# Optimization experiments

Measured on AMD Instinct MI355X. Metric: run time of the kernel, lower is better.

Reference implementation:

```python
import jax, jax.numpy as jnp
import numpy as np

TW, NV, EMB, LAYERS = 25, 4, 128, 6
N, E = 65536, 262144
T_MAX = 16.0
EPS = 1e-5

def silu(x):
    return x * jax.nn.sigmoid(x)

def setup_inputs() -> dict:
    key = jax.random.key(0)
    ks = iter(jax.random.split(key, 32))
    def nrm(shape, scale=0.05):
        return jax.random.normal(next(ks), shape, jnp.float32) * scale
    inp = {}
    inp['x'] = jax.random.normal(next(ks), (N, TW), jnp.float32)
    inp['pos'] = jax.random.uniform(next(ks), (N, 1), jnp.float32)
    inp['variables'] = jax.random.uniform(next(ks), (N, NV), jnp.float32)
    inp['dt'] = jnp.full((1,), 0.1, jnp.float32)
    inp['edge_index'] = jax.random.randint(next(ks), (2, E), 0, N)
    inp['enc_W1'] = nrm((TW + NV + 1, EMB)); inp['enc_b1'] = jnp.zeros((EMB,), jnp.float32)
    inp['enc_W2'] = nrm((EMB, EMB));         inp['enc_b2'] = jnp.zeros((EMB,), jnp.float32)
    dmsg = 2 * EMB + TW + 1 + NV   # 286: x_i,x_j,u_i-u_j,pos_i-pos_j,vars_i
    dupd = 2 * EMB + NV            # 260: x, aggregated message, vars
    inp['msg_W1'] = nrm((LAYERS, dmsg, EMB)); inp['msg_b1'] = jnp.zeros((LAYERS, EMB), jnp.float32)
    inp['msg_W2'] = nrm((LAYERS, EMB, EMB));  inp['msg_b2'] = jnp.zeros((LAYERS, EMB), jnp.float32)
    inp['upd_W1'] = nrm((LAYERS, dupd, EMB)); inp['upd_b1'] = jnp.zeros((LAYERS, EMB), jnp.float32)
    inp['upd_W2'] = nrm((LAYERS, EMB, EMB));  inp['upd_b2'] = jnp.zeros((LAYERS, EMB), jnp.float32)
    inp['dec_W1'] = nrm((8, 1, 16)); inp['dec_b1'] = jnp.zeros((8,), jnp.float32)
    inp['dec_W2'] = nrm((1, 8, 14)); inp['dec_b2'] = jnp.zeros((1,), jnp.float32)
    return inp

def reference(x, pos, variables, dt, edge_index,
              enc_W1, enc_b1, enc_W2, enc_b2,
              msg_W1, msg_b1, msg_W2, msg_b2,
              upd_W1, upd_b1, upd_W2, upd_b2,
              dec_W1, dec_b1, dec_W2, dec_b2):
    vars3 = variables[:, :3]              # alpha, beta, gamma
    t = variables[:, 3:4] / T_MAX         # normalized time
    p = pos / jnp.max(pos)                # graph.pos /= pos.max()
    inp0 = jnp.concatenate([x, p, t, vars3], axis=-1)  # [N, 30]
    h = silu(silu(inp0 @ enc_W1 + enc_b1) @ enc_W2 + enc_b2)  # [N, EMB]

    src, dst = edge_index[0], edge_index[1]  # x_j = src, x_i = dst (source_to_target)
    deg = jax.ops.segment_sum(jnp.ones((E,), jnp.float32), dst, num_segments=N)
    inv_deg = (1.0 / jnp.maximum(deg, 1.0))[:, None]

    for l in range(LAYERS):
        m_in = jnp.concatenate(
            [h[dst], h[src], x[dst] - x[src], p[dst] - p[src], variables[dst]], axis=-1)
        m = silu(m_in @ msg_W1[l] + msg_b1[l])
        m = silu(m @ msg_W2[l] + msg_b2[l])                      # [E, EMB]
        agg = jax.ops.segment_sum(m, dst, num_segments=N) * inv_deg  # mean aggr
        u = silu(jnp.concatenate([h, agg, variables], axis=-1) @ upd_W1[l] + upd_b1[l])
        u = silu(u @ upd_W2[l] + upd_b2[l])
        h_new = h + u  # in_features == out_features -> residual
        # PyG InstanceNorm (affine=False), single graph (batch all zeros)
        mu = jnp.mean(h_new, axis=0, keepdims=True)
        var = jnp.var(h_new, axis=0, keepdims=True)
        h = (h_new - mu) * jax.lax.rsqrt(var + EPS)

    # decoder: Conv1d(1->8, k=16, s=3) -> SiLU -> Conv1d(8->1, k=14, s=1)
    z = h[:, None, :]  # [N, 1, EMB]
    z = jax.lax.conv_general_dilated(z, dec_W1, (3,), 'VALID',
                                     dimension_numbers=('NCH', 'OIH', 'NCH')) + dec_b1[None, :, None]
    z = silu(z)
    z = jax.lax.conv_general_dilated(z, dec_W2, (1,), 'VALID',
                                     dimension_numbers=('NCH', 'OIH', 'NCH')) + dec_b2[None, :, None]
    diff = z[:, 0, :]  # [N, TW]
    dtc = dt[0] * jnp.arange(1, TW + 1, dtype=jnp.float32)  # cumsum of dt*ones
    return jnp.tile(x[:, -1:], (1, TW)) + dtc[None, :] * diff
```

## Files before the change

### kernel.cpp

```cpp
#include <hip/hip_runtime.h>
#include <math.h>

#define N_NODES 65536
#define N_EDGES 262144
#define N_LAYERS 6
#define T_MAX_F 16.0f
#define EPS_F 1e-5f

typedef float  f32x4  __attribute__((ext_vector_type(4)));
typedef __bf16 bf16x8 __attribute__((ext_vector_type(8)));
typedef __bf16 bf16x4 __attribute__((ext_vector_type(4)));

__device__ __forceinline__ float silu_f(float v){
    return v / (1.0f + __expf(-v));
}

__device__ __forceinline__ f32x4 mfma16(bf16x8 a, bf16x8 b, f32x4 c){
    return __builtin_amdgcn_mfma_f32_16x16x32_bf16(a, b, c, 0, 0, 0);
}

#define PK_RA (6 * 20480)
#define PK_RB (6 * 20480)
#define PK_M2 (6 * 16384)
#define PK_U1 (6 * 36864)
#define PK_U2 (6 * 16384)
#define PK_TOTAL (PK_RA + PK_RB + PK_M2 + PK_U1 + PK_U2)

__global__ __launch_bounds__(256) void k_pack(const float* __restrict__ msgW1, const float* __restrict__ msgW2,
                                              const float* __restrict__ updW1, const float* __restrict__ updW2,
                                              __bf16* __restrict__ out){
    int pg = blockIdx.x * 256 + threadIdx.x;
    if (pg >= PK_TOTAL) return;
    int p = pg;
    int mode; const float* W; int perL;
    if (p < PK_RA){ mode = 0; W = msgW1; perL = 20480; }
    else if ((p -= PK_RA) < PK_RB){ mode = 1; W = msgW1; perL = 20480; }
    else if ((p -= PK_RB) < PK_M2){ mode = 2; W = msgW2; perL = 16384; }
    else if ((p -= PK_M2) < PK_U1){ mode = 3; W = updW1; perL = 36864; }
    else { p -= PK_U1; mode = 4; W = updW2; perL = 16384; }
    int l = p / perL, q = p % perL;
    int elem = q & 7, lane = (q >> 3) & 63, cb = (q >> 9) & 7, kb = q >> 12;
    int col = cb * 16 + (lane & 15);
    int k = kb * 32 + ((lane >> 4) << 3) + elem;
    float v = 0.0f;
    if (mode == 0){
        int r = -1;
        if (k < 128) r = k;
        else if (k < 153) r = 256 + (k - 128);
        else if (k == 153) r = 281;
        else if (k < 158) r = 282 + (k - 154);
        if (r >= 0) v = W[(size_t)l * 286 * 128 + (size_t)r * 128 + col];
    } else if (mode == 1){
        if (k < 128) v = W[(size_t)l * 286 * 128 + (size_t)(128 + k) * 128 + col];
        else if (k < 153) v = -W[(size_t)l * 286 * 128 + (size_t)(256 + (k - 128)) * 128 + col];
        else if (k == 153) v = -W[(size_t)l * 286 * 128 + (size_t)281 * 128 + col];
    } else {
        int Kreal = (mode == 3) ? 260 : 128;
        if (k < Kreal) v = W[(size_t)l * Kreal * 128 + (size_t)k * 128 + col];
    }
    out[pg] = (__bf16)v;
}

__global__ __launch_bounds__(256) void k_max(const float* __restrict__ pos, unsigned* __restrict__ outmax){
    __shared__ float s[256];
    int tid = threadIdx.x;
    float m = 0.0f;
    for (int i = blockIdx.x * 256 + tid; i < N_NODES; i += 256 * 256)
        m = fmaxf(m, pos[i]);
    s[tid] = m;
    __syncthreads();
    for (int off = 128; off > 0; off >>= 1){
        if (tid < off) s[tid] = fmaxf(s[tid], s[tid + off]);
        __syncthreads();
    }
    if (tid == 0) atomicMax(outmax, __float_as_uint(s[0]));
}

__global__ __launch_bounds__(256) void k_deg(const int* __restrict__ dst, int* __restrict__ deg){
    int i = blockIdx.x * 256 + threadIdx.x;
    if (i < N_EDGES) atomicAdd(deg + dst[i], 1);
}

__global__ __launch_bounds__(256) void k_prep(const float* __restrict__ pos, const unsigned* __restrict__ maxp,
                                              const int* __restrict__ deg,
                                              float* __restrict__ p, float* __restrict__ invdeg){
    int i = blockIdx.x * 256 + threadIdx.x;
    if (i < N_NODES){
        float mp = __uint_as_float(*maxp);
        p[i] = pos[i] / mp;
        invdeg[i] = 1.0f / fmaxf((float)deg[i], 1.0f);
    }
}

__global__ __launch_bounds__(256) void k_scan1(const int* __restrict__ deg, int* __restrict__ csum){
    __shared__ int s[256];
    int c = blockIdx.x, t = threadIdx.x;
    s[t] = deg[c * 256 + t];
    __syncthreads();
    for (int o = 128; o > 0; o >>= 1){ if (t < o) s[t] += s[t + o]; __syncthreads(); }
    if (t == 0) csum[c] = s[0];
}

__global__ __launch_bounds__(256) void k_scan2(const int* __restrict__ csum, int* __restrict__ coff){
    __shared__ int s[256];
    int t = threadIdx.x;
    s[t] = csum[t];
    __syncthreads();
    for (int o = 1; o < 256; o <<= 1){
        int v = (t >= o) ? s[t - o] : 0;
        __syncthreads();
        s[t] += v;
        __syncthreads();
    }
    coff[t] = s[t] - csum[t];
}

__global__ __launch_bounds__(256) void k_scan3(const int* __restrict__ deg, const int* __restrict__ coff,
                                               int* __restrict__ cursor){
    __shared__ int s[256];
    int c = blockIdx.x, t = threadIdx.x;
    int d = deg[c * 256 + t];
    s[t] = d;
    __syncthreads();
    for (int o = 1; o < 256; o <<= 1){
        int v = (t >= o) ? s[t - o] : 0;
        __syncthreads();
        s[t] += v;
        __syncthreads();
    }
    cursor[c * 256 + t] = coff[c] + s[t] - d;
}

__global__ __launch_bounds__(256) void k_scatter(const int* __restrict__ esrc, const int* __restrict__ edst,
                                                 int* __restrict__ cursor,
                                                 int* __restrict__ ssrcS, int* __restrict__ sdstS){
    int e = blockIdx.x * 256 + threadIdx.x;
    if (e < N_EDGES){
        int d = edst[e];
        int slot = atomicAdd(cursor + d, 1);
        ssrcS[slot] = esrc[e];
        sdstS[slot] = d;
    }
}

__device__ __forceinline__ void gemm44(const float* A, int lda, const float* __restrict__ W,
                                       int kq_begin, int kq_end, int r0, int c0, float acc[4][4]){
    for (int kq = kq_begin; kq < kq_end; ++kq){
        int k = kq * 4;
        float a[4][4], w[4][4];
        #pragma unroll
        for (int i = 0; i < 4; ++i){
            float4 v = *(const float4*)(A + (r0 + i) * lda + k);
            a[i][0] = v.x; a[i][1] = v.y; a[i][2] = v.z; a[i][3] = v.w;
        }
        #pragma unroll
        for (int kk = 0; kk < 4; ++kk){
            float4 v = *(const float4*)(W + (k + kk) * 128 + c0);
            w[kk][0] = v.x; w[kk][1] = v.y; w[kk][2] = v.z; w[kk][3] = v.w;
        }
        #pragma unroll
        for (int kk = 0; kk < 4; ++kk)
            #pragma unroll
            for (int i = 0; i < 4; ++i)
                #pragma unroll
                for (int j = 0; j < 4; ++j)
                    acc[i][j] = fmaf(a[i][kk], w[kk][j], acc[i][j]);
    }
}

__global__ __launch_bounds__(256) void k_enc(const float* __restrict__ x, const float* __restrict__ p,
                                             const float* __restrict__ vars,
                                             const float* __restrict__ W1, const float* __restrict__ b1,
                                             const float* __restrict__ W2, const float* __restrict__ b2,
                                             float* __restrict__ hA){
    __shared__ __align__(16) float sin_[32 * 32];
    __shared__ __align__(16) float sw1[32 * 128];
    __shared__ __align__(16) float sy[32 * 128];
    int tid = threadIdx.x;
    int n0 = blockIdx.x * 32;
    for (int i = tid; i < 32 * 32; i += 256){
        int e = i >> 5, k = i & 31;
        int node = n0 + e;
        float v;
        if (k < 25)       v = x[node * 25 + k];
        else if (k == 25) v = p[node];
        else if (k == 26) v = vars[node * 4 + 3] * (1.0f / T_MAX_F);
        else if (k < 30)  v = vars[node * 4 + (k - 27)];
        else              v = 0.0f;
        sin_[e * 32 + k] = v;
    }
    for (int i = tid; i < 32 * 128; i += 256){
        int r = i >> 7;
        sw1[i] = (r < 30) ? W1[i] : 0.0f;
    }
    __syncthreads();
    int c0 = (tid & 31) * 4, r0 = (tid >> 5) * 4;
    float acc[4][4] = {};
    gemm44(sin_, 32, sw1, 0, 8, r0, c0, acc);
    float4 bv = *(const float4*)(b1 + c0);
    float b_[4] = {bv.x, bv.y, bv.z, bv.w};
    #pragma unroll
    for (int i = 0; i < 4; ++i){
        float4 o;
        o.x = silu_f(acc[i][0] + b_[0]);
        o.y = silu_f(acc[i][1] + b_[1]);
        o.z = silu_f(acc[i][2] + b_[2]);
        o.w = silu_f(acc[i][3] + b_[3]);
        *(float4*)(sy + (r0 + i) * 128 + c0) = o;
    }
    __syncthreads();
    float acc2[4][4] = {};
    gemm44(sy, 128, W2, 0, 32, r0, c0, acc2);
    float4 b2v = *(const float4*)(b2 + c0);
    float bb[4] = {b2v.x, b2v.y, b2v.z, b2v.w};
    #pragma unroll
    for (int i = 0; i < 4; ++i){
        float4 o;
        o.x = silu_f(acc2[i][0] + bb[0]);
        o.y = silu_f(acc2[i][1] + bb[1]);
        o.z = silu_f(acc2[i][2] + bb[2]);
        o.w = silu_f(acc2[i][3] + bb[3]);
        *(float4*)(hA + (size_t)(n0 + r0 + i) * 128 + c0) = o;
    }
}

__global__ __launch_bounds__(256) void k_npre(const float* __restrict__ hA, const float* __restrict__ x,
                                              const float* __restrict__ p, const float* __restrict__ vars,
                                              const float* __restrict__ mu, const float* __restrict__ istd,
                                              int apply_ln,
                                              const __bf16* __restrict__ Wra, const __bf16* __restrict__ Wrb,
                                              const float* __restrict__ b1,
                                              float* __restrict__ raO, __bf16* __restrict__ rbO,
                                              float* __restrict__ aggZ, float* __restrict__ saccZ){
    __shared__ __align__(16) __bf16 sA[10 * 64 * 8];
    __shared__ __align__(16) float sOut[32 * 264];
    int tid = threadIdx.x;
    int n0 = blockIdx.x * 32;
    {
        float4 z4 = {0.f, 0.f, 0.f, 0.f};
        #pragma unroll
        for (int it = 0; it < 4; ++it){
            int i = tid + it * 256;
            int e = i >> 5, ch = i & 31;
            *(float4*)(aggZ + (size_t)(n0 + e) * 128 + ch * 4) = z4;
        }
        if (blockIdx.x == 0) saccZ[tid] = 0.f;
    }
    #pragma unroll
    for (int it = 0; it < 3; ++it){
        int j = tid + it * 256;
        if (j < 640){
            int f = j >> 6, lane = j & 63;
            int kb = f >> 1, mt = f & 1;
            int e = (lane & 15) + mt * 16, kh = lane >> 4;
            int node = n0 + e;
            bf16x8 o;
            if (kb < 4){
                int k0 = kb * 32 + kh * 8;
                float4 v0 = *(const float4*)(hA + (size_t)node * 128 + k0);
                float4 v1 = *(const float4*)(hA + (size_t)node * 128 + k0 + 4);
                if (apply_ln){
                    float4 m0 = *(const float4*)(mu + k0),   m1 = *(const float4*)(mu + k0 + 4);
                    float4 s0 = *(const float4*)(istd + k0), s1 = *(const float4*)(istd + k0 + 4);
                    v0.x = (v0.x - m0.x) * s0.x; v0.y = (v0.y - m0.y) * s0.y;
                    v0.z = (v0.z - m0.z) * s0.z; v0.w = (v0.w - m0.w) * s0.w;
                    v1.x = (v1.x - m1.x) * s1.x; v1.y = (v1.y - m1.y) * s1.y;
                    v1.z = (v1.z - m1.z) * s1.z; v1.w = (v1.w - m1.w) * s1.w;
                }
                o[0] = (__bf16)v0.x; o[1] = (__bf16)v0.y; o[2] = (__bf16)v0.z; o[3] = (__bf16)v0.w;
                o[4] = (__bf16)v1.x; o[5] = (__bf16)v1.y; o[6] = (__bf16)v1.z; o[7] = (__bf16)v1.w;
            } else {
                #pragma unroll
                for (int jj = 0; jj < 8; ++jj){
                    int fk = kh * 8 + jj;
                    float v;
                    if (fk < 25)       v = x[node * 25 + fk];
                    else if (fk == 25) v = p[node];
                    else if (fk < 30)  v = vars[node * 4 + (fk - 26)];
                    else               v = 0.0f;
                    o[jj] = (__bf16)v;
                }
            }
            *(bf16x8*)(sA + (f * 64 + lane) * 8) = o;
        }
    }
    __syncthreads();
    int w = tid >> 6, lane = tid & 63;
    int clo = lane & 15, rhi = lane >> 4;
    f32x4 z = {0.f, 0.f, 0.f, 0.f};
    f32x4 aR[2][2] = {{z, z}, {z, z}};
    f32x4 aB[2][2] = {{z, z}, {z, z}};
    #pragma unroll
    for (int kb = 0; kb < 5; ++kb){
        bf16x8 a0 = *(bf16x8*)(sA + ((kb * 2 + 0) * 64 + lane) * 8);
        bf16x8 a1 = *(bf16x8*)(sA + ((kb * 2 + 1) * 64 + lane) * 8);
        bf16x8 wr0 = *(const bf16x8*)(Wra + (size_t)((kb * 8 + 2 * w)     * 64 + lane) * 8);
        bf16x8 wr1 = *(const bf16x8*)(Wra + (size_t)((kb * 8 + 2 * w + 1) * 64 + lane) * 8);
        bf16x8 wb0 = *(const bf16x8*)(Wrb + (size_t)((kb * 8 + 2 * w)     * 64 + lane) * 8);
        bf16x8 wb1 = *(const bf16x8*)(Wrb + (size_t)((kb * 8 + 2 * w + 1) * 64 + lane) * 8);
        aR[0][0] = mfma16(a0, wr0, aR[0][0]);
        aR[0][1] = mfma16(a0, wr1, aR[0][1]);
        aR[1][0] = mfma16(a1, wr0, aR[1][0]);
        aR[1][1] = mfma16(a1, wr1, aR[1][1]);
        aB[0][0] = mfma16(a0, wb0, aB[0][0]);
        aB[0][1] = mfma16(a0, wb1, aB[0][1]);
        aB[1][0] = mfma16(a1, wb0, aB[1][0]);
        aB[1][1] = mfma16(a1, wb1, aB[1][1]);
    }
    #pragma unroll
    for (int nf = 0; nf < 2; ++nf){
        int col = (2 * w + nf) * 16 + clo;
        float bv = b1[col];
        #pragma unroll
        for (int mt = 0; mt < 2; ++mt)
            #pragma unroll
            for (int i = 0; i < 4; ++i){
                int e = mt * 16 + rhi * 4 + i;
                sOut[e * 264 + col]       = aR[mt][nf][i] + bv;
                sOut[e * 264 + 128 + col] = aB[mt][nf][i];
            }
    }
    __syncthreads();
    #pragma unroll
    for (int it = 0; it < 4; ++it){
        int j = tid + it * 256;
        int row = j >> 5, c8 = j & 31;
        const float* src = sOut + row * 264 + c8 * 8;
        if (c8 < 16){
            float4 v0 = *(const float4*)(src);
            float4 v1 = *(const float4*)(src + 4);
            float* dstp = raO + (size_t)(n0 + row) * 128 + c8 * 8;
            *(float4*)(dstp)     = v0;
            *(float4*)(dstp + 4) = v1;
        } else {
            bf16x8 o;
            #pragma unroll
            for (int t = 0; t < 8; ++t) o[t] = (__bf16)src[t];
            *(bf16x8*)(rbO + (size_t)(n0 + row) * 128 + (c8 - 16) * 8) = o;
        }
    }
}

__global__ __launch_bounds__(256) void k_edge3(const float* __restrict__ ra, const __bf16* __restrict__ rb,
                                               const int* __restrict__ ssrcS, const int* __restrict__ sdstS,
                                               const __bf16* __restrict__ Wp2, const float* __restrict__ bias2,
                                               float* __restrict__ agg){
    __shared__ __align__(16) unsigned char smem[64 * 128 * 4];
    __shared__ int sd[64], ss[64];
    __bf16* sA   = (__bf16*)smem;
    float*  msum = (float*)smem;
    int tid = threadIdx.x;
    int e0 = blockIdx.x * 64;
    if (tid < 64){ sd[tid] = sdstS[e0 + tid]; ss[tid] = ssrcS[e0 + tid]; }
    __syncthreads();
    #pragma unroll
    for (int it = 0; it < 4; ++it){
        int j = tid + it * 256;
        int f = j >> 6, lane = j & 63;
        int kb = f >> 2, mt = f & 3;
        int e = (lane & 15) + mt * 16;
        int k0 = kb * 32 + (lane >> 4) * 8;
        const float* rap = ra + (size_t)sd[e] * 128 + k0;
        float4 v0 = *(const float4*)(rap);
        float4 v1 = *(const float4*)(rap + 4);
        bf16x8 vb = *(const bf16x8*)(rb + (size_t)ss[e] * 128 + k0);
        bf16x8 o;
        o[0] = (__bf16)silu_f(v0.x + (float)vb[0]);
        o[1] = (__bf16)silu_f(v0.y + (float)vb[1]);
        o[2] = (__bf16)silu_f(v0.z + (float)vb[2]);
        o[3] = (__bf16)silu_f(v0.w + (float)vb[3]);
        o[4] = (__bf16)silu_f(v1.x + (float)vb[4]);
        o[5] = (__bf16)silu_f(v1.y + (float)vb[5]);
        o[6] = (__bf16)silu_f(v1.z + (float)vb[6]);
        o[7] = (__bf16)silu_f(v1.w + (float)vb[7]);
        *(bf16x8*)(sA + (f * 64 + lane) * 8) = o;
    }
    __syncthreads();
    int w = tid >> 6, lane = tid & 63;
    int cb0 = 2 * w, clo = lane & 15, rhi = lane >> 4;
    f32x4 z = {0.f, 0.f, 0.f, 0.f};
    f32x4 acc[4][2] = {{z, z}, {z, z}, {z, z}, {z, z}};
    #pragma unroll
    for (int kb = 0; kb < 4; ++kb){
        bf16x8 a0 = *(bf16x8*)(sA + ((kb * 4 + 0) * 64 + lane) * 8);
        bf16x8 a1 = *(bf16x8*)(sA + ((kb * 4 + 1) * 64 + lane) * 8);
        bf16x8 a2 = *(bf16x8*)(sA + ((kb * 4 + 2) * 64 + lane) * 8);
        bf16x8 a3 = *(bf16x8*)(sA + ((kb * 4 + 3) * 64 + lane) * 8);
        bf16x8 w0 = *(const bf16x8*)(Wp2 + (size_t)((kb * 8 + cb0)     * 64 + lane) * 8);
        bf16x8 w1 = *(const bf16x8*)(Wp2 + (size_t)((kb * 8 + cb0 + 1) * 64 + lane) * 8);
        acc[0][0] = mfma16(a0, w0, acc[0][0]);
        acc[0][1] = mfma16(a0, w1, acc[0][1]);
        acc[1][0] = mfma16(a1, w0, acc[1][0]);
        acc[1][1] = mfma16(a1, w1, acc[1][1]);
        acc[2][0] = mfma16(a2, w0, acc[2][0]);
        acc[2][1] = mfma16(a2, w1, acc[2][1]);
        acc[3][0] = mfma16(a3, w0, acc[3][0]);
        acc[3][1] = mfma16(a3, w1, acc[3][1]);
    }
    __syncthreads();
    #pragma unroll
    for (int nf = 0; nf < 2; ++nf){
        int col = (cb0 + nf) * 16 + clo;
        float bv = bias2[col];
        #pragma unroll
        for (int mt = 0; mt < 4; ++mt)
            #pragma unroll
            for (int i = 0; i < 4; ++i){
                int row = mt * 16 + rhi * 4 + i;
                msum[row * 128 + col] = silu_f(acc[mt][nf][i] + bv);
            }
    }
    __syncthreads();
    int col = tid & 127, half = tid >> 7;
    int base = half * 32;
    float run = 0.0f;
    for (int r = 0; r < 32; ++r){
        int row = base + r;
        run += msum[row * 128 + col];
        bool flush = (r == 31) || (sd[row + 1] != sd[row]);
        if (flush){
            atomicAdd(agg + (size_t)sd[row] * 128 + col, run);
            run = 0.0f;
        }
    }
}

__global__ __launch_bounds__(256) void k_upd_m(float* __restrict__ hA, const float* __restrict__ agg,
                                               const float* __restrict__ vars, const float* __restrict__ invdeg,
                                               const float* __restrict__ mu, const float* __restrict__ istd,
                                               int apply_ln,
                                               const __bf16* __restrict__ Wp1, const float* __restrict__ bias1,
                                               const __bf16* __restrict__ Wp2, const float* __restrict__ bias2,
                                               float* __restrict__ sacc, float* __restrict__ qacc){
    __shared__ __align__(16) __bf16 sA1[36 * 64 * 8];
    __bf16* zb = sA1;
    int tid = threadIdx.x;
    int n0 = blockIdx.x * 64;
    #pragma unroll
    for (int it = 0; it < 9; ++it){
        int idx = tid + it * 256;
        int f = idx >> 6, lane = idx & 63;
        int kb = f >> 2, mt = f & 3;
        int row = (lane & 15) + mt * 16;
        int node = n0 + row;
        int k0 = kb * 32 + ((lane >> 4) << 3);
        bf16x8 o;
        if (k0 < 128){
            float4 v0 = *(const float4*)(hA + (size_t)node * 128 + k0);
            float4 v1 = *(const float4*)(hA + (size_t)node * 128 + k0 + 4);
            if (apply_ln){
                float4 m0 = *(const float4*)(mu + k0),   m1 = *(const float4*)(mu + k0 + 4);
                float4 s0 = *(const float4*)(istd + k0), s1 = *(const float4*)(istd + k0 + 4);
                v0.x = (v0.x - m0.x) * s0.x; v0.y = (v0.y - m0.y) * s0.y;
                v0.z = (v0.z - m0.z) * s0.z; v0.w = (v0.w - m0.w) * s0.w;
                v1.x = (v1.x - m1.x) * s1.x; v1.y = (v1.y - m1.y) * s1.y;
                v1.z = (v1.z - m1.z) * s1.z; v1.w = (v1.w - m1.w) * s1.w;
            }
            o[0] = (__bf16)v0.x; o[1] = (__bf16)v0.y; o[2] = (__bf16)v0.z; o[3] = (__bf16)v0.w;
            o[4] = (__bf16)v1.x; o[5] = (__bf16)v1.y; o[6] = (__bf16)v1.z; o[7] = (__bf16)v1.w;
        } else if (k0 < 256){
            int g0 = k0 - 128;
            float4 v0 = *(const float4*)(agg + (size_t)node * 128 + g0);
            float4 v1 = *(const float4*)(agg + (size_t)node * 128 + g0 + 4);
            float s = invdeg[node];
            o[0] = (__bf16)(v0.x * s); o[1] = (__bf16)(v0.y * s); o[2] = (__bf16)(v0.z * s); o[3] = (__bf16)(v0.w * s);
            o[4] = (__bf16)(v1.x * s); o[5] = (__bf16)(v1.y * s); o[6] = (__bf16)(v1.z * s); o[7] = (__bf16)(v1.w * s);
        } else {
            int fk = k0 - 256;
            #pragma unroll
            for (int jj = 0; jj < 8; ++jj){
                int kk = fk + jj;
                o[jj] = (__bf16)((kk < 4) ? vars[(size_t)node * 4 + kk] : 0.0f);
            }
        }
        *(bf16x8*)(sA1 + (size_t)idx * 8) = o;
    }
    __syncthreads();
    int w = tid >> 6, lane = tid & 63;
    int cb0 = 2 * w, clo = lane & 15, rhi = lane >> 4;
    f32x4 z = {0.f, 0.f, 0.f, 0.f};
    f32x4 acc[4][2] = {{z, z}, {z, z}, {z, z}, {z, z}};
    #pragma unroll
    for (int kb = 0; kb < 9; ++kb){
        bf16x8 w0 = *(const bf16x8*)(Wp1 + (size_t)((kb * 8 + cb0)     * 64 + lane) * 8);
        bf16x8 w1 = *(const bf16x8*)(Wp1 + (size_t)((kb * 8 + cb0 + 1) * 64 + lane) * 8);
        #pragma unroll
        for (int mt = 0; mt < 4; ++mt){
            bf16x8 a = *(bf16x8*)(sA1 + ((kb * 4 + mt) * 64 + lane) * 8);
            acc[mt][0] = mfma16(a, w0, acc[mt][0]);
            acc[mt][1] = mfma16(a, w1, acc[mt][1]);
        }
    }
    __syncthreads();
    #pragma unroll
    for (int nf = 0; nf < 2; ++nf){
        int col = (cb0 + nf) * 16 + clo;
        float bv = bias1[col];
        #pragma unroll
        for (int mt = 0; mt < 4; ++mt)
            #pragma unroll
            for (int i = 0; i < 4; ++i){
                int row = mt * 16 + rhi * 4 + i;
                zb[row * 152 + col] = (__bf16)silu_f(acc[mt][nf][i] + bv);
            }
    }
    __syncthreads();
    f32x4 acc2[4][2] = {{z, z}, {z, z}, {z, z}, {z, z}};
    #pragma unroll
    for (int kb = 0; kb < 4; ++kb){
        bf16x8 w0 = *(const bf16x8*)(Wp2 + (size_t)((kb * 8 + cb0)     * 64 + lane) * 8);
        bf16x8 w1 = *(const bf16x8*)(Wp2 + (size_t)((kb * 8 + cb0 + 1) * 64 + lane) * 8);
        int k0 = kb * 32 + ((lane >> 4) << 3);
        #pragma unroll
        for (int mt = 0; mt < 4; ++mt){
            int row = (lane & 15) + mt * 16;
            bf16x8 a = *(bf16x8*)(zb + row * 152 + k0);
            acc2[mt][0] = mfma16(a, w0, acc2[mt][0]);
            acc2[mt][1] = mfma16(a, w1, acc2[mt][1]);
        }
    }
    float sm[2] = {0.f, 0.f}, sq[2] = {0.f, 0.f};
    #pragma unroll
    for (int nf = 0; nf < 2; ++nf){
        int col = (cb0 + nf) * 16 + clo;
        float bv = bias2[col];
        float muv = apply_ln ? mu[col] : 0.0f;
        float sdv = apply_ln ? istd[col] : 1.0f;
        #pragma unroll
        for (int mt = 0; mt < 4; ++mt)
            #pragma unroll
            for (int i = 0; i < 4; ++i){
                int row = mt * 16 + rhi * 4 + i;
                size_t idx = (size_t)(n0 + row) * 128 + col;
                float u = silu_f(acc2[mt][nf][i] + bv);
                float hln = (hA[idx] - muv) * sdv;
                float hv = hln + u;
                hA[idx] = hv;
                sm[nf] += hv; sq[nf] += hv * hv;
            }
    }
    #pragma unroll
    for (int nf = 0; nf < 2; ++nf){
        float s = sm[nf], q = sq[nf];
        s += __shfl_xor(s, 16); q += __shfl_xor(q, 16);
        s += __shfl_xor(s, 32); q += __shfl_xor(q, 32);
        if (rhi == 0){
            int col = (cb0 + nf) * 16 + clo;
            atomicAdd(sacc + col, s);
            atomicAdd(qacc + col, q);
        }
    }
}

__global__ __launch_bounds__(128) void k_statfin(const float* __restrict__ sacc, const float* __restrict__ qacc,
                                                 float* __restrict__ mu, float* __restrict__ istd){
    int c = threadIdx.x;
    float m = sacc[c] * (1.0f / N_NODES);
    float v = qacc[c] * (1.0f / N_NODES) - m * m;
    mu[c] = m;
    istd[c] = rsqrtf(v + EPS_F);
}

#define DECNB 16
__global__ __launch_bounds__(256) void k_dec(const float* __restrict__ h, const float* __restrict__ x,
                                             const float* __restrict__ dt,
                                             const float* __restrict__ W1, const float* __restrict__ b1,
                                             const float* __restrict__ W2, const float* __restrict__ b2,
                                             const float* __restrict__ mu, const float* __restrict__ istd,
                                             float* __restrict__ out){
    __shared__ __align__(16) float sh[DECNB * 132];
    __shared__ __align__(16) float so[DECNB * 312];
    __shared__ float pp[DECNB * 8 * 26];
    __shared__ float sw1[128], sw2[112], sb1[8];
    int tid = threadIdx.x;
    int n0 = blockIdx.x * DECNB;
    for (int i = tid; i < DECNB * 32; i += 256){
        int g = i >> 5, chunk = i & 31;
        float4 v = *(const float4*)(h + (size_t)(n0 + g) * 128 + chunk * 4);
        float4 m = *(const float4*)(mu + chunk * 4);
        float4 s = *(const float4*)(istd + chunk * 4);
        v.x = (v.x - m.x) * s.x; v.y = (v.y - m.y) * s.y;
        v.z = (v.z - m.z) * s.z; v.w = (v.w - m.w) * s.w;
        *(float4*)(sh + g * 132 + chunk * 4) = v;
    }
    if (tid < 128) sw1[tid] = W1[tid];
    else if (tid < 240) sw2[tid - 128] = W2[tid - 128];
    if (tid < 8) sb1[tid] = b1[tid];
    __syncthreads();
    {
        int g = tid >> 4, c = (tid >> 1) & 7, jh = tid & 1;
        int j0 = jh * 19;
        float w[16];
        #pragma unroll
        for (int k = 0; k < 16; ++k) w[k] = sw1[c * 16 + k];
        float bc = sb1[c];
        float win[16];
        #pragma unroll
        for (int k = 0; k < 16; ++k) win[k] = sh[g * 132 + 3 * j0 + k];
        #pragma unroll
        for (int j = 0; j < 19; ++j){
            float a = bc;
            #pragma unroll
            for (int k = 0; k < 16; ++k) a = fmaf(win[k], w[k], a);
            so[g * 312 + c * 38 + j0 + j] = silu_f(a);
            if (j < 18){
                #pragma unroll
                for (int k = 0; k < 13; ++k) win[k] = win[k + 3];
                int base = g * 132 + 3 * (j0 + j + 1) + 13;
                win[13] = sh[base]; win[14] = sh[base + 1]; win[15] = sh[base + 2];
            }
        }
    }
    __syncthreads();
    {
        int g = tid >> 4, c = (tid >> 1) & 7, th = tid & 1;
        int t0 = th * 13;
        int nt = th ? 12 : 13;
        float w[14];
        #pragma unroll
        for (int k = 0; k < 14; ++k) w[k] = sw2[c * 14 + k];
        float win[14];
        #pragma unroll
        for (int k = 0; k < 14; ++k) win[k] = so[g * 312 + c * 38 + t0 + k];
        #pragma unroll
        for (int t = 0; t < 13; ++t){
            if (t < nt){
                float a = 0.0f;
                #pragma unroll
                for (int k = 0; k < 14; ++k) a = fmaf(win[k], w[k], a);
                pp[(g * 8 + c) * 26 + t0 + t] = a;
            }
            if (t + 1 < nt){
                #pragma unroll
                for (int k = 0; k < 13; ++k) win[k] = win[k + 1];
                win[13] = so[g * 312 + c * 38 + t0 + t + 14];
            }
        }
    }
    __syncthreads();
    float dtv = dt[0];
    for (int i = tid; i < DECNB * 25; i += 256){
        int g = i / 25, t = i % 25;
        float a = b2[0];
        #pragma unroll
        for (int c = 0; c < 8; ++c) a += pp[(g * 8 + c) * 26 + t];
        out[(size_t)(n0 + g) * 25 + t] = x[(size_t)(n0 + g) * 25 + 24] + dtv * (float)(t + 1) * a;
    }
}

extern "C" void kernel_launch(void* const* d_in, const int* in_sizes, int n_in,
                              void* d_out, int out_size, void* d_ws, size_t ws_size,
                              hipStream_t stream){
    (void)in_sizes; (void)n_in; (void)out_size; (void)ws_size;
    const float* x      = (const float*)d_in[0];
    const float* pos    = (const float*)d_in[1];
    const float* vars   = (const float*)d_in[2];
    const float* dt     = (const float*)d_in[3];
    const int*   ei     = (const int*)d_in[4];
    const float* encW1  = (const float*)d_in[5];
    const float* encb1  = (const float*)d_in[6];
    const float* encW2  = (const float*)d_in[7];
    const float* encb2  = (const float*)d_in[8];
    const float* msgW1  = (const float*)d_in[9];
    const float* msgb1  = (const float*)d_in[10];
    const float* msgW2  = (const float*)d_in[11];
    const float* msgb2  = (const float*)d_in[12];
    const float* updW1  = (const float*)d_in[13];
    const float* updb1  = (const float*)d_in[14];
    const float* updW2  = (const float*)d_in[15];
    const float* updb2  = (const float*)d_in[16];
    const float* decW1  = (const float*)d_in[17];
    const float* decb1  = (const float*)d_in[18];
    const float* decW2  = (const float*)d_in[19];
    const float* decb2  = (const float*)d_in[20];
    float* out = (float*)d_out;

    float* ws = (float*)d_ws;
    size_t off = 0;
    float* hA      = ws + off; off += (size_t)N_NODES * 128;
    float* agg     = ws + off; off += (size_t)N_NODES * 128;
    float* sacc    = ws + off; off += 128;
    float* qacc    = ws + off; off += 128;
    float* raF     = ws + off; off += (size_t)N_NODES * 128;
    float* p       = ws + off; off += N_NODES;
    float* invdeg  = ws + off; off += N_NODES;
    float* muArr   = ws + off; off += 6 * 128;
    float* istdArr = ws + off; off += 6 * 128;
    int* deg       = (int*)(ws + off); off += N_NODES;
    unsigned* maxp = (unsigned*)(ws + off); off += 2;
    int* csum      = (int*)(ws + off); off += 256;
    int* coff      = (int*)(ws + off); off += 256;
    int* cursor    = (int*)(ws + off); off += N_NODES;
    int* ssrcS     = (int*)(ws + off); off += N_EDGES;
    int* sdstS     = (int*)(ws + off); off += N_EDGES;
    __bf16* wpack  = (__bf16*)(ws + off); off += (PK_TOTAL + 1) / 2;
    __bf16* rbB    = (__bf16*)(ws + off); off += (size_t)N_NODES * 64;

    __bf16* pra = wpack;
    __bf16* prb = pra + PK_RA;
    __bf16* pm2 = prb + PK_RB;
    __bf16* pu1 = pm2 + PK_M2;
    __bf16* pu2 = pu1 + PK_U1;

    const int* esrc = ei;
    const int* edst = ei + N_EDGES;

    hipMemsetAsync(deg, 0, (size_t)N_NODES * sizeof(int) + sizeof(unsigned), stream);

    k_pack<<<(PK_TOTAL + 255) / 256, 256, 0, stream>>>(msgW1, msgW2, updW1, updW2, wpack);
    k_max<<<256, 256, 0, stream>>>(pos, maxp);
    k_deg<<<N_EDGES / 256, 256, 0, stream>>>(edst, deg);
    k_scan1<<<256, 256, 0, stream>>>(deg, csum);
    k_scan2<<<1, 256, 0, stream>>>(csum, coff);
    k_scan3<<<256, 256, 0, stream>>>(deg, coff, cursor);
    k_scatter<<<N_EDGES / 256, 256, 0, stream>>>(esrc, edst, cursor, ssrcS, sdstS);
    k_prep<<<N_NODES / 256, 256, 0, stream>>>(pos, maxp, deg, p, invdeg);
    k_enc<<<N_NODES / 32, 256, 0, stream>>>(x, p, vars, encW1, encb1, encW2, encb2, hA);

    for (int l = 0; l < N_LAYERS; ++l){
        const float* muPrev   = (l > 0) ? (muArr + (size_t)(l - 1) * 128) : muArr;
        const float* istdPrev = (l > 0) ? (istdArr + (size_t)(l - 1) * 128) : istdArr;
        k_npre<<<N_NODES / 32, 256, 0, stream>>>(hA, x, p, vars, muPrev, istdPrev, (l > 0) ? 1 : 0,
            pra + (size_t)l * 20480, prb + (size_t)l * 20480, msgb1 + l * 128, raF, rbB, agg, sacc);
        k_edge3<<<N_EDGES / 64, 256, 0, stream>>>(raF, rbB, ssrcS, sdstS,
            pm2 + (size_t)l * 16384, msgb2 + l * 128, agg);
        k_upd_m<<<N_NODES / 64, 256, 0, stream>>>(hA, agg, vars, invdeg, muPrev, istdPrev, (l > 0) ? 1 : 0,
            pu1 + (size_t)l * 36864, updb1 + l * 128,
            pu2 + (size_t)l * 16384, updb2 + l * 128, sacc, qacc);
        k_statfin<<<1, 128, 0, stream>>>(sacc, qacc, muArr + (size_t)l * 128, istdArr + (size_t)l * 128);
    }

    k_dec<<<N_NODES / DECNB, 256, 0, stream>>>(hA, x, dt, decW1, decb1, decW2, decb2,
                                               muArr + 5 * 128, istdArr + 5 * 128, out);
}
```

Baseline: 920.7 us.

## Fuse setup kernels, drop stat-finalize kernel, store ra half in bf16

Merges the degree count with the pos max reduction, and the edge scatter with the p/invdeg prep, cutting two launches. The per-layer statistics finalize kernel is removed: each consumer kernel now computes mean and rsqrt variance from double-buffered sum and sum-of-squares arrays into shared memory. The dst-side message precompute (ra) is stored as bf16 instead of fp32, which halves its write in k_npre and its gather in k_edge3 at some cost in precision. The stat buffer alternates by layer parity; the decoder reads slot 1, which is the one written by layer 5.

```diff
diff --git a/kernel.cpp b/kernel.cpp
--- a/kernel.cpp
+++ b/kernel.cpp
@@ -9,7 +9,6 @@
 
 typedef float  f32x4  __attribute__((ext_vector_type(4)));
 typedef __bf16 bf16x8 __attribute__((ext_vector_type(8)));
-typedef __bf16 bf16x4 __attribute__((ext_vector_type(4)));
 
 __device__ __forceinline__ float silu_f(float v){
     return v / (1.0f + __expf(-v));
@@ -61,34 +60,20 @@
     out[pg] = (__bf16)v;
 }
 
-__global__ __launch_bounds__(256) void k_max(const float* __restrict__ pos, unsigned* __restrict__ outmax){
+__global__ __launch_bounds__(256) void k_deg_max(const int* __restrict__ dst, const float* __restrict__ pos,
+                                                 int* __restrict__ deg, unsigned* __restrict__ outmax){
     __shared__ float s[256];
     int tid = threadIdx.x;
-    float m = 0.0f;
-    for (int i = blockIdx.x * 256 + tid; i < N_NODES; i += 256 * 256)
-        m = fmaxf(m, pos[i]);
-    s[tid] = m;
-    __syncthreads();
-    for (int off = 128; off > 0; off >>= 1){
-        if (tid < off) s[tid] = fmaxf(s[tid], s[tid + off]);
+    int e = blockIdx.x * 256 + tid;
+    if (e < N_EDGES) atomicAdd(deg + dst[e], 1);
+    if (blockIdx.x < N_NODES / 256){
+        s[tid] = pos[blockIdx.x * 256 + tid];
         __syncthreads();
-    }
-    if (tid == 0) atomicMax(outmax, __float_as_uint(s[0]));
-}
-
-__global__ __launch_bounds__(256) void k_deg(const int* __restrict__ dst, int* __restrict__ deg){
-    int i = blockIdx.x * 256 + threadIdx.x;
-    if (i < N_EDGES) atomicAdd(deg + dst[i], 1);
-}
-
-__global__ __launch_bounds__(256) void k_prep(const float* __restrict__ pos, const unsigned* __restrict__ maxp,
-                                              const int* __restrict__ deg,
-                                              float* __restrict__ p, float* __restrict__ invdeg){
-    int i = blockIdx.x * 256 + threadIdx.x;
-    if (i < N_NODES){
-        float mp = __uint_as_float(*maxp);
-        p[i] = pos[i] / mp;
-        invdeg[i] = 1.0f / fmaxf((float)deg[i], 1.0f);
+        for (int off = 128; off > 0; off >>= 1){
+            if (tid < off) s[tid] = fmaxf(s[tid], s[tid + off]);
+            __syncthreads();
+        }
+        if (tid == 0) atomicMax(outmax, __float_as_uint(s[0]));
     }
 }
 
@@ -131,15 +116,24 @@
     cursor[c * 256 + t] = coff[c] + s[t] - d;
 }
 
-__global__ __launch_bounds__(256) void k_scatter(const int* __restrict__ esrc, const int* __restrict__ edst,
-                                                 int* __restrict__ cursor,
-                                                 int* __restrict__ ssrcS, int* __restrict__ sdstS){
+__global__ __launch_bounds__(256) void k_scatter_prep(const int* __restrict__ esrc, const int* __restrict__ edst,
+                                                      int* __restrict__ cursor,
+                                                      int* __restrict__ ssrcS, int* __restrict__ sdstS,
+                                                      const float* __restrict__ pos, const unsigned* __restrict__ maxp,
+                                                      const int* __restrict__ deg,
+                                                      float* __restrict__ p, float* __restrict__ invdeg){
     int e = blockIdx.x * 256 + threadIdx.x;
     if (e < N_EDGES){
         int d = edst[e];
         int slot = atomicAdd(cursor + d, 1);
         ssrcS[slot] = esrc[e];
         sdstS[slot] = d;
+    }
+    if (blockIdx.x < N_NODES / 256){
+        int i = blockIdx.x * 256 + threadIdx.x;
+        float mp = __uint_as_float(*maxp);
+        p[i] = pos[i] / mp;
+        invdeg[i] = 1.0f / fmaxf((float)deg[i], 1.0f);
     }
 }
 
@@ -226,16 +220,23 @@
 
 __global__ __launch_bounds__(256) void k_npre(const float* __restrict__ hA, const float* __restrict__ x,
                                               const float* __restrict__ p, const float* __restrict__ vars,
-                                              const float* __restrict__ mu, const float* __restrict__ istd,
-                                              int apply_ln,
+                                              const float* __restrict__ statPrev, int apply_ln,
                                               const __bf16* __restrict__ Wra, const __bf16* __restrict__ Wrb,
                                               const float* __restrict__ b1,
-                                              float* __restrict__ raO, __bf16* __restrict__ rbO,
-                                              float* __restrict__ aggZ, float* __restrict__ saccZ){
+                                              __bf16* __restrict__ raO, __bf16* __restrict__ rbO,
+                                              float* __restrict__ aggZ, float* __restrict__ statCurZ){
     __shared__ __align__(16) __bf16 sA[10 * 64 * 8];
     __shared__ __align__(16) float sOut[32 * 264];
+    __shared__ __align__(16) float smu[128], sistd[128];
     int tid = threadIdx.x;
     int n0 = blockIdx.x * 32;
+    if (apply_ln && tid < 128){
+        float m = statPrev[tid] * (1.0f / N_NODES);
+        float v = statPrev[128 + tid] * (1.0f / N_NODES) - m * m;
+        smu[tid] = m;
+        sistd[tid] = rsqrtf(v + EPS_F);
+    }
+    if (blockIdx.x == 0) statCurZ[tid] = 0.f;
     {
         float4 z4 = {0.f, 0.f, 0.f, 0.f};
         #pragma unroll
@@ -244,8 +245,8 @@
             int e = i >> 5, ch = i & 31;
             *(float4*)(aggZ + (size_t)(n0 + e) * 128 + ch * 4) = z4;
         }
-        if (blockIdx.x == 0) saccZ[tid] = 0.f;
-    }
+    }
+    __syncthreads();
     #pragma unroll
     for (int it = 0; it < 3; ++it){
         int j = tid + it * 256;
@@ -260,8 +261,8 @@
                 float4 v0 = *(const float4*)(hA + (size_t)node * 128 + k0);
                 float4 v1 = *(const float4*)(hA + (size_t)node * 128 + k0 + 4);
                 if (apply_ln){
-                    float4 m0 = *(const float4*)(mu + k0),   m1 = *(const float4*)(mu + k0 + 4);
-                    float4 s0 = *(const float4*)(istd + k0), s1 = *(const float4*)(istd + k0 + 4);
+                    float4 m0 = *(const float4*)(smu + k0),   m1 = *(const float4*)(smu + k0 + 4);
+                    float4 s0 = *(const float4*)(sistd + k0), s1 = *(const float4*)(sistd + k0 + 4);
                     v0.x = (v0.x - m0.x) * s0.x; v0.y = (v0.y - m0.y) * s0.y;
                     v0.z = (v0.z - m0.z) * s0.z; v0.w = (v0.w - m0.w) * s0.w;
                     v1.x = (v1.x - m1.x) * s1.x; v1.y = (v1.y - m1.y) * s1.y;
@@ -326,22 +327,16 @@
         int j = tid + it * 256;
         int row = j >> 5, c8 = j & 31;
         const float* src = sOut + row * 264 + c8 * 8;
-        if (c8 < 16){
-            float4 v0 = *(const float4*)(src);
-            float4 v1 = *(const float4*)(src + 4);
-            float* dstp = raO + (size_t)(n0 + row) * 128 + c8 * 8;
-            *(float4*)(dstp)     = v0;
-            *(float4*)(dstp + 4) = v1;
-        } else {
-            bf16x8 o;
-            #pragma unroll
-            for (int t = 0; t < 8; ++t) o[t] = (__bf16)src[t];
-            *(bf16x8*)(rbO + (size_t)(n0 + row) * 128 + (c8 - 16) * 8) = o;
-        }
-    }
-}
-
-__global__ __launch_bounds__(256) void k_edge3(const float* __restrict__ ra, const __bf16* __restrict__ rb,
+        bf16x8 o;
+        #pragma unroll
+        for (int t = 0; t < 8; ++t) o[t] = (__bf16)src[t];
+        __bf16* dstp = (c8 < 16) ? (raO + (size_t)(n0 + row) * 128 + c8 * 8)
+                                 : (rbO + (size_t)(n0 + row) * 128 + (c8 - 16) * 8);
+        *(bf16x8*)dstp = o;
+    }
+}
+
+__global__ __launch_bounds__(256) void k_edge3(const __bf16* __restrict__ ra, const __bf16* __restrict__ rb,
                                                const int* __restrict__ ssrcS, const int* __restrict__ sdstS,
                                                const __bf16* __restrict__ Wp2, const float* __restrict__ bias2,
                                                float* __restrict__ agg){
@@ -360,19 +355,12 @@
         int kb = f >> 2, mt = f & 3;
         int e = (lane & 15) + mt * 16;
         int k0 = kb * 32 + (lane >> 4) * 8;
-        const float* rap = ra + (size_t)sd[e] * 128 + k0;
-        float4 v0 = *(const float4*)(rap);
-        float4 v1 = *(const float4*)(rap + 4);
+        bf16x8 va = *(const bf16x8*)(ra + (size_t)sd[e] * 128 + k0);
         bf16x8 vb = *(const bf16x8*)(rb + (size_t)ss[e] * 128 + k0);
         bf16x8 o;
-        o[0] = (__bf16)silu_f(v0.x + (float)vb[0]);
-        o[1] = (__bf16)silu_f(v0.y + (float)vb[1]);
-        o[2] = (__bf16)silu_f(v0.z + (float)vb[2]);
-        o[3] = (__bf16)silu_f(v0.w + (float)vb[3]);
-        o[4] = (__bf16)silu_f(v1.x + (float)vb[4]);
-        o[5] = (__bf16)silu_f(v1.y + (float)vb[5]);
-        o[6] = (__bf16)silu_f(v1.z + (float)vb[6]);
-        o[7] = (__bf16)silu_f(v1.w + (float)vb[7]);
+        #pragma unroll
+        for (int t = 0; t < 8; ++t)
+            o[t] = (__bf16)silu_f((float)va[t] + (float)vb[t]);
         *(bf16x8*)(sA + (f * 64 + lane) * 8) = o;
     }
     __syncthreads();
@@ -427,15 +415,22 @@
 
 __global__ __launch_bounds__(256) void k_upd_m(float* __restrict__ hA, const float* __restrict__ agg,
                                                const float* __restrict__ vars, const float* __restrict__ invdeg,
-                                               const float* __restrict__ mu, const float* __restrict__ istd,
-                                               int apply_ln,
+                                               const float* __restrict__ statPrev, int apply_ln,
                                                const __bf16* __restrict__ Wp1, const float* __restrict__ bias1,
                                                const __bf16* __restrict__ Wp2, const float* __restrict__ bias2,
-                                               float* __restrict__ sacc, float* __restrict__ qacc){
+                                               float* __restrict__ statCur){
     __shared__ __align__(16) __bf16 sA1[36 * 64 * 8];
+    __shared__ __align__(16) float smu[128], sistd[128];
     __bf16* zb = sA1;
     int tid = threadIdx.x;
     int n0 = blockIdx.x * 64;
+    if (apply_ln && tid < 128){
+        float m = statPrev[tid] * (1.0f / N_NODES);
+        float v = statPrev[128 + tid] * (1.0f / N_NODES) - m * m;
+        smu[tid] = m;
+        sistd[tid] = rsqrtf(v + EPS_F);
+    }
+    __syncthreads();
     #pragma unroll
     for (int it = 0; it < 9; ++it){
         int idx = tid + it * 256;
@@ -449,8 +444,8 @@
             float4 v0 = *(const float4*)(hA + (size_t)node * 128 + k0);
             float4 v1 = *(const float4*)(hA + (size_t)node * 128 + k0 + 4);
             if (apply_ln){
-                float4 m0 = *(const float4*)(mu + k0),   m1 = *(const float4*)(mu + k0 + 4);
-                float4 s0 = *(const float4*)(istd + k0), s1 = *(const float4*)(istd + k0 + 4);
+                float4 m0 = *(const float4*)(smu + k0),   m1 = *(const float4*)(smu + k0 + 4);
+                float4 s0 = *(const float4*)(sistd + k0), s1 = *(const float4*)(sistd + k0 + 4);
                 v0.x = (v0.x - m0.x) * s0.x; v0.y = (v0.y - m0.y) * s0.y;
                 v0.z = (v0.z - m0.z) * s0.z; v0.w = (v0.w - m0.w) * s0.w;
                 v1.x = (v1.x - m1.x) * s1.x; v1.y = (v1.y - m1.y) * s1.y;
@@ -524,8 +519,8 @@
     for (int nf = 0; nf < 2; ++nf){
         int col = (cb0 + nf) * 16 + clo;
         float bv = bias2[col];
-        float muv = apply_ln ? mu[col] : 0.0f;
-        float sdv = apply_ln ? istd[col] : 1.0f;
+        float muv = apply_ln ? smu[col] : 0.0f;
+        float sdv = apply_ln ? sistd[col] : 1.0f;
         #pragma unroll
         for (int mt = 0; mt < 4; ++mt)
             #pragma unroll
@@ -546,19 +541,10 @@
         s += __shfl_xor(s, 32); q += __shfl_xor(q, 32);
         if (rhi == 0){
             int col = (cb0 + nf) * 16 + clo;
-            atomicAdd(sacc + col, s);
-            atomicAdd(qacc + col, q);
-        }
-    }
-}
-
-__global__ __launch_bounds__(128) void k_statfin(const float* __restrict__ sacc, const float* __restrict__ qacc,
-                                                 float* __restrict__ mu, float* __restrict__ istd){
-    int c = threadIdx.x;
-    float m = sacc[c] * (1.0f / N_NODES);
-    float v = qacc[c] * (1.0f / N_NODES) - m * m;
-    mu[c] = m;
-    istd[c] = rsqrtf(v + EPS_F);
+            atomicAdd(statCur + col, s);
+            atomicAdd(statCur + 128 + col, q);
+        }
+    }
 }
 
 #define DECNB 16
@@ -566,26 +552,33 @@
                                              const float* __restrict__ dt,
                                              const float* __restrict__ W1, const float* __restrict__ b1,
                                              const float* __restrict__ W2, const float* __restrict__ b2,
-                                             const float* __restrict__ mu, const float* __restrict__ istd,
+                                             const float* __restrict__ statPrev,
                                              float* __restrict__ out){
     __shared__ __align__(16) float sh[DECNB * 132];
     __shared__ __align__(16) float so[DECNB * 312];
     __shared__ float pp[DECNB * 8 * 26];
     __shared__ float sw1[128], sw2[112], sb1[8];
+    __shared__ __align__(16) float smu[128], sistd[128];
     int tid = threadIdx.x;
     int n0 = blockIdx.x * DECNB;
+    if (tid < 128){
+        float m = statPrev[tid] * (1.0f / N_NODES);
+        float v = statPrev[128 + tid] * (1.0f / N_NODES) - m * m;
+        smu[tid] = m;
+        sistd[tid] = rsqrtf(v + EPS_F);
+        sw1[tid] = W1[tid];
+    } else if (tid < 240) sw2[tid - 128] = W2[tid - 128];
+    if (tid < 8) sb1[tid] = b1[tid];
+    __syncthreads();
     for (int i = tid; i < DECNB * 32; i += 256){
         int g = i >> 5, chunk = i & 31;
         float4 v = *(const float4*)(h + (size_t)(n0 + g) * 128 + chunk * 4);
-        float4 m = *(const float4*)(mu + chunk * 4);
-        float4 s = *(const float4*)(istd + chunk * 4);
+        float4 m = *(const float4*)(smu + chunk * 4);
+        float4 s = *(const float4*)(sistd + chunk * 4);
         v.x = (v.x - m.x) * s.x; v.y = (v.y - m.y) * s.y;
         v.z = (v.z - m.z) * s.z; v.w = (v.w - m.w) * s.w;
         *(float4*)(sh + g * 132 + chunk * 4) = v;
     }
-    if (tid < 128) sw1[tid] = W1[tid];
-    else if (tid < 240) sw2[tid - 128] = W2[tid - 128];
-    if (tid < 8) sb1[tid] = b1[tid];
     __syncthreads();
     {
         int g = tid >> 4, c = (tid >> 1) & 7, jh = tid & 1;
@@ -679,13 +672,9 @@
     size_t off = 0;
     float* hA      = ws + off; off += (size_t)N_NODES * 128;
     float* agg     = ws + off; off += (size_t)N_NODES * 128;
-    float* sacc    = ws + off; off += 128;
-    float* qacc    = ws + off; off += 128;
-    float* raF     = ws + off; off += (size_t)N_NODES * 128;
+    float* sstat   = ws + off; off += 2 * 256;
     float* p       = ws + off; off += N_NODES;
     float* invdeg  = ws + off; off += N_NODES;
-    float* muArr   = ws + off; off += 6 * 128;
-    float* istdArr = ws + off; off += 6 * 128;
     int* deg       = (int*)(ws + off); off += N_NODES;
     unsigned* maxp = (unsigned*)(ws + off); off += 2;
     int* csum      = (int*)(ws + off); off += 256;
@@ -694,6 +683,7 @@
     int* ssrcS     = (int*)(ws + off); off += N_EDGES;
     int* sdstS     = (int*)(ws + off); off += N_EDGES;
     __bf16* wpack  = (__bf16*)(ws + off); off += (PK_TOTAL + 1) / 2;
+    __bf16* raB    = (__bf16*)(ws + off); off += (size_t)N_NODES * 64;
     __bf16* rbB    = (__bf16*)(ws + off); off += (size_t)N_NODES * 64;
 
     __bf16* pra = wpack;
@@ -708,28 +698,28 @@
     hipMemsetAsync(deg, 0, (size_t)N_NODES * sizeof(int) + sizeof(unsigned), stream);
 
     k_pack<<<(PK_TOTAL + 255) / 256, 256, 0, stream>>>(msgW1, msgW2, updW1, updW2, wpack);
-    k_max<<<256, 256, 0, stream>>>(pos, maxp);
-    k_deg<<<N_EDGES / 256, 256, 0, stream>>>(edst, deg);
+    k_deg_max<<<N_EDGES / 256, 256, 0, stream>>>(edst, pos, deg, maxp);
     k_scan1<<<256, 256, 0, stream>>>(deg, csum);
     k_scan2<<<1, 256, 0, stream>>>(csum, coff);
     k_scan3<<<256, 256, 0, stream>>>(deg, coff, cursor);
-    k_scatter<<<N_EDGES / 256, 256, 0, stream>>>(esrc, edst, cursor, ssrcS, sdstS);
-    k_prep<<<N_NODES / 256, 256, 0, stream>>>(pos, maxp, deg, p, invdeg);
+    k_scatter_prep<<<N_EDGES / 256, 256, 0, stream>>>(esrc, edst, cursor, ssrcS, sdstS,
+                                                      pos, maxp, deg, p, invdeg);
     k_enc<<<N_NODES / 32, 256, 0, stream>>>(x, p, vars, encW1, encb1, encW2, encb2, hA);
 
     for (int l = 0; l < N_LAYERS; ++l){
-        const float* muPrev   = (l > 0) ? (muArr + (size_t)(l - 1) * 128) : muArr;
-        const float* istdPrev = (l > 0) ? (istdArr + (size_t)(l - 1) * 128) : istdArr;
-        k_npre<<<N_NODES / 32, 256, 0, stream>>>(hA, x, p, vars, muPrev, istdPrev, (l > 0) ? 1 : 0,
-            pra + (size_t)l * 20480, prb + (size_t)l * 20480, msgb1 + l * 128, raF, rbB, agg, sacc);
-        k_edge3<<<N_EDGES / 64, 256, 0, stream>>>(raF, rbB, ssrcS, sdstS,
+        int cur = l & 1;
+        float* statCur        = sstat + (size_t)cur * 256;
+        const float* statPrev = sstat + (size_t)(cur ^ 1) * 256;
+        k_npre<<<N_NODES / 32, 256, 0, stream>>>(hA, x, p, vars, statPrev, (l > 0) ? 1 : 0,
+            pra + (size_t)l * 20480, prb + (size_t)l * 20480, msgb1 + l * 128,
+            raB, rbB, agg, statCur);
+        k_edge3<<<N_EDGES / 64, 256, 0, stream>>>(raB, rbB, ssrcS, sdstS,
             pm2 + (size_t)l * 16384, msgb2 + l * 128, agg);
-        k_upd_m<<<N_NODES / 64, 256, 0, stream>>>(hA, agg, vars, invdeg, muPrev, istdPrev, (l > 0) ? 1 : 0,
+        k_upd_m<<<N_NODES / 64, 256, 0, stream>>>(hA, agg, vars, invdeg, statPrev, (l > 0) ? 1 : 0,
             pu1 + (size_t)l * 36864, updb1 + l * 128,
-            pu2 + (size_t)l * 16384, updb2 + l * 128, sacc, qacc);
-        k_statfin<<<1, 128, 0, stream>>>(sacc, qacc, muArr + (size_t)l * 128, istdArr + (size_t)l * 128);
+            pu2 + (size_t)l * 16384, updb2 + l * 128, statCur);
     }
 
     k_dec<<<N_NODES / DECNB, 256, 0, stream>>>(hA, x, dt, decW1, decb1, decW2, decb2,
-                                               muArr + 5 * 128, istdArr + 5 * 128, out);
-}
+                                               sstat + 256, out);
+}
```

New measurement: 878.5 us, median of 3. -4.6%, faster.
